# Kernel tuning notes

Hardware: AMD Instinct MI355X
Metric: run time of the kernel (lower is better)

## Reference

```python
import jax, jax.numpy as jnp
import numpy as np

N = 50000
NEG_SLOPE = 0.2  # PyG GATConv default negative_slope


def gat_conv(x, src, dst, W, a_src, a_dst, bias, concat):
    """One PyG-style GATConv (eval mode, self-loops already in src/dst).
    x: [N, F_in], W: [F_in, H*C], a_src/a_dst: [H, C], bias: [H*C] or [C].
    """
    H, C = a_src.shape
    xl = (x @ W).reshape(N, H, C)                      # [N, H, C]
    alpha_src = jnp.sum(xl * a_src, axis=-1)           # [N, H]
    alpha_dst = jnp.sum(xl * a_dst, axis=-1)           # [N, H]
    e = jax.nn.leaky_relu(alpha_src[src] + alpha_dst[dst], NEG_SLOPE)  # [E, H]
    # edge-softmax over incoming edges of each destination node
    m = jax.ops.segment_max(e, dst, num_segments=N)    # [N, H]
    e = jnp.exp(e - m[dst])
    s = jax.ops.segment_sum(e, dst, num_segments=N)    # [N, H]
    alpha = e / s[dst]                                 # [E, H]
    msg = xl[src] * alpha[:, :, None]                  # [E, H, C]
    out = jax.ops.segment_sum(msg, dst, num_segments=N)  # [N, H, C]
    out = out.reshape(N, H * C) if concat else out.mean(axis=1)
    return out + bias


def setup_inputs() -> dict:
    key = jax.random.key(0)
    ks = jax.random.split(key, 10)
    in_ch, hid, out_ch, heads = 128, 64, 64, 4
    E = 800000
    x = jax.random.normal(ks[0], (N, in_ch), dtype=jnp.float32)
    edge_index = jax.random.randint(ks[1], (2, E), 0, N, dtype=jnp.int64)
    s1 = 1.0 / np.sqrt(in_ch)
    s2 = 1.0 / np.sqrt(hid * heads)
    return {
        "x": x,
        "edge_index": edge_index,
        "W1": jax.random.normal(ks[2], (in_ch, heads * hid), jnp.float32) * s1,
        "att_src1": jax.random.normal(ks[3], (heads, hid), jnp.float32) * s1,
        "att_dst1": jax.random.normal(ks[4], (heads, hid), jnp.float32) * s1,
        "b1": jnp.zeros((heads * hid,), jnp.float32),
        "W2": jax.random.normal(ks[5], (heads * hid, out_ch), jnp.float32) * s2,
        "att_src2": jax.random.normal(ks[6], (1, out_ch), jnp.float32) * s2,
        "att_dst2": jax.random.normal(ks[7], (1, out_ch), jnp.float32) * s2,
        "b2": jnp.zeros((out_ch,), jnp.float32),
    }


def reference(x, edge_index, W1, att_src1, att_dst1, b1, W2, att_src2, att_dst2, b2):
    # PyG GATConv adds self-loops by default
    loops = jnp.arange(N, dtype=edge_index.dtype)
    src = jnp.concatenate([edge_index[0], loops])
    dst = jnp.concatenate([edge_index[1], loops])
    h = gat_conv(x, src, dst, W1, att_src1, att_dst1, b1, concat=True)
    h = jax.nn.elu(h)  # dropout is identity in eval mode
    out = gat_conv(h, src, dst, W2, att_src2, att_dst2, b2, concat=False)
    return out
```

## Files before the change

kernel.cpp:

```cpp
#include <hip/hip_runtime.h>
#include <math.h>


typedef unsigned short u16;
typedef short s8v __attribute__((ext_vector_type(8)));
typedef float f32x4 __attribute__((ext_vector_type(4)));

#define LOG2E 1.4426950408889634f

__device__ __forceinline__ float bflo(unsigned int u) {
  return __builtin_bit_cast(float, u << 16);
}
__device__ __forceinline__ float bfhi(unsigned int u) {
  return __builtin_bit_cast(float, u & 0xffff0000u);
}
__device__ __forceinline__ u16 f2bf(float f) {
  unsigned int u = __builtin_bit_cast(unsigned int, f);
  return (u16)((u + 0x7fff + ((u >> 16) & 1)) >> 16);
}


__global__ void prep_count_kernel(const int* __restrict__ ei, int E, int Nn,
                                  int* __restrict__ deg,
                                  const float* __restrict__ W1, u16* __restrict__ W1T,
                                  const float* __restrict__ W2, u16* __restrict__ W2T) {
  int i = blockIdx.x * blockDim.x + threadIdx.x;
  int Et = E + Nn;
  if (i < Et) {
    int dst = (i < E) ? ei[E + i] : (i - E);
    atomicAdd(&deg[dst], 1);
    return;
  }
  int e = i - Et;
  if (e < 128 * 256) {
    int k = e >> 8, n = e & 255;
    W1T[n * 128 + k] = f2bf(W1[e]);
    return;
  }
  e -= 128 * 256;
  if (e < 256 * 64) {
    int k = e >> 6, n = e & 63;
    W2T[n * 256 + k] = f2bf(W2[e]);
  }
}

__global__ void scan_partials_kernel(const int* __restrict__ deg,
                                     int* __restrict__ partials, int Ntot) {
  __shared__ int red[256];
  int t = threadIdx.x;
  int base = blockIdx.x * 1024 + t * 4;
  int s = 0;
  if (base + 3 < Ntot) {
    int4 v = *(const int4*)(deg + base);
    s = v.x + v.y + v.z + v.w;
  } else {
    for (int i = 0; i < 4; ++i)
      if (base + i < Ntot) s += deg[base + i];
  }
  red[t] = s;
  __syncthreads();
  for (int off = 128; off > 0; off >>= 1) {
    if (t < off) red[t] += red[t + off];
    __syncthreads();
  }
  if (t == 0) partials[blockIdx.x] = red[0];
}

__global__ void scan_final_kernel(const int* __restrict__ deg,
                                  const int* __restrict__ partials,
                                  int* __restrict__ rowptr,
                                  int* __restrict__ cursor, int Ntot, int NB) {
  __shared__ int sums[256];
  int t = threadIdx.x;
  int bid = blockIdx.x;
  int base = bid * 1024 + t * 4;
  int4 v = make_int4(0, 0, 0, 0);
  if (base + 3 < Ntot) {
    v = *(const int4*)(deg + base);
  } else {
    if (base + 0 < Ntot) v.x = deg[base + 0];
    if (base + 1 < Ntot) v.y = deg[base + 1];
    if (base + 2 < Ntot) v.z = deg[base + 2];
    if (base + 3 < Ntot) v.w = deg[base + 3];
  }
  sums[t] = v.x + v.y + v.z + v.w;
  __syncthreads();
  for (int off = 1; off < 256; off <<= 1) {
    int u = (t >= off) ? sums[t - off] : 0;
    __syncthreads();
    sums[t] += u;
    __syncthreads();
  }
  int boff = 0;
  for (int j = 0; j < bid; ++j) boff += partials[j];
  int excl = boff + ((t == 0) ? 0 : sums[t - 1]);
  int4 r;
  r.x = excl;
  r.y = r.x + v.x;
  r.z = r.y + v.y;
  r.w = r.z + v.z;
  if (base + 3 < Ntot) {
    *(int4*)(rowptr + base) = r;
    *(int4*)(cursor + base) = r;
  } else {
    if (base + 0 < Ntot) { rowptr[base + 0] = r.x; cursor[base + 0] = r.x; }
    if (base + 1 < Ntot) { rowptr[base + 1] = r.y; cursor[base + 1] = r.y; }
    if (base + 2 < Ntot) { rowptr[base + 2] = r.z; cursor[base + 2] = r.z; }
    if (base + 3 < Ntot) { rowptr[base + 3] = r.w; cursor[base + 3] = r.w; }
  }
}

__global__ void scatter_edges_kernel(const int* __restrict__ ei, int E, int Nn,
                                     int* __restrict__ cursor, int* __restrict__ col) {
  int e = blockIdx.x * blockDim.x + threadIdx.x;
  if (e >= E + Nn) return;
  int src, dst;
  if (e < E) { src = ei[e]; dst = ei[E + e]; }
  else       { src = dst = e - E; }
  int pos = atomicAdd(&cursor[dst], 1);
  col[pos] = src;
}


__global__ __launch_bounds__(256) void gemm1_fused_kernel(
    const float* __restrict__ x,
    const u16* __restrict__ w1t,
    const float* __restrict__ a_src,
    const float* __restrict__ a_dst,
    u16* __restrict__ C,
    float* __restrict__ asrc, float* __restrict__ adst,
    int M) {
  constexpr int BM = 128, BN = 128, BK = 32, PK = 40;
  __shared__ short As[BM][PK];
  __shared__ short Bs[BN][PK];
  int tid = threadIdx.x;
  int lane = tid & 63, w = tid >> 6;
  int q = lane >> 4, fr = lane & 15;
  int wm = (w >> 1) * 64, wn = (w & 1) * 64;
  int bm0 = blockIdx.x * BM, bn0 = blockIdx.y * BN;
  int fk = q * 8;

  f32x4 acc[4][4] = {};

  for (int k0 = 0; k0 < 128; k0 += BK) {
#pragma unroll
    for (int p = 0; p < 4; ++p) {
      int idx = p * 1024 + tid * 4;
      int r = idx >> 5, c = idx & 31;
      float4 v = make_float4(0.f, 0.f, 0.f, 0.f);
      if (bm0 + r < M) v = *(const float4*)(x + (size_t)(bm0 + r) * 128 + k0 + c);
      *(ushort4*)&As[r][c] = make_ushort4(f2bf(v.x), f2bf(v.y), f2bf(v.z), f2bf(v.w));
    }
#pragma unroll
    for (int p = 0; p < 2; ++p) {
      int idx = p * 2048 + tid * 8;
      int r = idx >> 5, c = idx & 31;
      *(s8v*)&Bs[r][c] = *(const s8v*)(w1t + (size_t)(bn0 + r) * 128 + k0 + c);
    }
    __syncthreads();

    s8v af[4], bf[4];
#pragma unroll
    for (int i = 0; i < 4; ++i)
      af[i] = *(const s8v*)&As[wm + i * 16 + fr][fk];
#pragma unroll
    for (int j = 0; j < 4; ++j)
      bf[j] = *(const s8v*)&Bs[wn + j * 16 + fr][fk];
#pragma unroll
    for (int i = 0; i < 4; ++i)
#pragma unroll
      for (int j = 0; j < 4; ++j)
        acc[i][j] = __builtin_amdgcn_mfma_f32_16x16x32_bf16(af[i], bf[j], acc[i][j], 0, 0, 0);
    __syncthreads();
  }

  int h = blockIdx.y * 2 + (wn >> 6);
  float asv[4], adv[4];
#pragma unroll
  for (int j = 0; j < 4; ++j) {
    asv[j] = a_src[h * 64 + j * 16 + fr];
    adv[j] = a_dst[h * 64 + j * 16 + fr];
  }
#pragma unroll
  for (int i = 0; i < 4; ++i) {
#pragma unroll
    for (int r = 0; r < 4; ++r) {
      int row = bm0 + wm + i * 16 + q * 4 + r;
      float ps = 0.f, pd = 0.f;
#pragma unroll
      for (int j = 0; j < 4; ++j) {
        ps = fmaf(acc[i][j][r], asv[j], ps);
        pd = fmaf(acc[i][j][r], adv[j], pd);
      }
#pragma unroll
      for (int mmask = 1; mmask < 16; mmask <<= 1) {
        ps += __shfl_xor(ps, mmask, 64);
        pd += __shfl_xor(pd, mmask, 64);
      }
      if (fr == 0 && row < M) {
        asrc[row * 4 + h] = ps * LOG2E;
        adst[row * 4 + h] = pd * LOG2E;
      }
    }
  }
#pragma unroll
  for (int i = 0; i < 4; ++i)
#pragma unroll
    for (int j = 0; j < 4; ++j)
#pragma unroll
      for (int r = 0; r < 4; ++r) {
        int row = bm0 + wm + i * 16 + q * 4 + r;
        if (row < M)
          C[(size_t)row * 256 + bn0 + wn + j * 16 + fr] = f2bf(acc[i][j][r]);
      }
}


__global__ __launch_bounds__(256) void gemm2_fused_kernel(
    const u16* __restrict__ A,
    const u16* __restrict__ Bt,
    const float* __restrict__ a_src,
    const float* __restrict__ a_dst,
    u16* __restrict__ C,
    float* __restrict__ asrc, float* __restrict__ adst,
    int M) {
  constexpr int BM = 128, BN = 64, BK = 32, PK = 40;
  __shared__ short As[BM][PK];
  __shared__ short Bs[BN][PK];
  __shared__ float alds[BM][4];
  int tid = threadIdx.x;
  int lane = tid & 63, w = tid >> 6;
  int q = lane >> 4, fr = lane & 15;
  int wm = (w >> 1) * 64, wn = (w & 1) * 32;
  int bm0 = blockIdx.x * BM;
  int fk = q * 8;

  f32x4 acc[4][2] = {};

  for (int k0 = 0; k0 < 256; k0 += BK) {
#pragma unroll
    for (int p = 0; p < 2; ++p) {
      int idx = p * 2048 + tid * 8;
      int r = idx / BK, c = idx % BK;
      *(s8v*)&As[r][c] = *(const s8v*)(A + (size_t)(bm0 + r) * 256 + k0 + c);
    }
    {
      int idx = tid * 8;
      int r = idx / BK, c = idx % BK;
      if (r < BN)
        *(s8v*)&Bs[r][c] = *(const s8v*)(Bt + (size_t)r * 256 + k0 + c);
    }
    __syncthreads();

    s8v af[4], bf[2];
#pragma unroll
    for (int i = 0; i < 4; ++i)
      af[i] = *(const s8v*)&As[wm + i * 16 + fr][fk];
#pragma unroll
    for (int j = 0; j < 2; ++j)
      bf[j] = *(const s8v*)&Bs[wn + j * 16 + fr][fk];
#pragma unroll
    for (int i = 0; i < 4; ++i)
#pragma unroll
      for (int j = 0; j < 2; ++j)
        acc[i][j] = __builtin_amdgcn_mfma_f32_16x16x32_bf16(af[i], bf[j], acc[i][j], 0, 0, 0);
    __syncthreads();
  }

  float asv[2], adv[2];
#pragma unroll
  for (int j = 0; j < 2; ++j) {
    asv[j] = a_src[wn + j * 16 + fr];
    adv[j] = a_dst[wn + j * 16 + fr];
  }
#pragma unroll
  for (int i = 0; i < 4; ++i) {
#pragma unroll
    for (int r = 0; r < 4; ++r) {
      int lr = wm + i * 16 + q * 4 + r;
      float ps = 0.f, pd = 0.f;
#pragma unroll
      for (int j = 0; j < 2; ++j) {
        ps = fmaf(acc[i][j][r], asv[j], ps);
        pd = fmaf(acc[i][j][r], adv[j], pd);
      }
#pragma unroll
      for (int mmask = 1; mmask < 16; mmask <<= 1) {
        ps += __shfl_xor(ps, mmask, 64);
        pd += __shfl_xor(pd, mmask, 64);
      }
      if (fr == 0) {
        alds[lr][(w & 1) * 2 + 0] = ps;
        alds[lr][(w & 1) * 2 + 1] = pd;
      }
    }
  }
#pragma unroll
  for (int i = 0; i < 4; ++i)
#pragma unroll
    for (int j = 0; j < 2; ++j)
#pragma unroll
      for (int r = 0; r < 4; ++r) {
        int row = bm0 + wm + i * 16 + q * 4 + r;
        if (row < M)
          C[(size_t)row * 64 + wn + j * 16 + fr] = f2bf(acc[i][j][r]);
      }
  __syncthreads();
  if (tid < BM) {
    int row = bm0 + tid;
    if (row < M) {
      asrc[row] = (alds[tid][0] + alds[tid][2]) * LOG2E;
      adst[row] = (alds[tid][1] + alds[tid][3]) * LOG2E;
    }
  }
}


__global__ void agg_multi_kernel(const u16* __restrict__ xlb,
                                 const float* __restrict__ asrc,
                                 const float* __restrict__ adst,
                                 const int* __restrict__ rowptr,
                                 const int* __restrict__ col,
                                 const float* __restrict__ bias,
                                 u16* __restrict__ hb, int Nn) {
  int n = blockIdx.x * 8 + (threadIdx.x >> 5);
  if (n >= Nn) return;
  int lane = threadIdx.x & 31;
  int h = lane >> 3;
  float adn = adst[n * 4 + h];
  int beg = rowptr[n], end = rowptr[n + 1];

  float s = 0.f;
  float acc[8] = {};

  float as0 = 0.f, as1 = 0.f, as2 = 0.f, as3 = 0.f;
  uint4 v0 = {}, v1 = {}, v2 = {}, v3 = {};
  {
    int sc = col[beg];
    as0 = asrc[sc * 4 + h];
    v0 = *(const uint4*)(xlb + (size_t)sc * 256 + lane * 8);
    if (beg + 1 < end) {
      int c1 = col[beg + 1];
      as1 = asrc[c1 * 4 + h];
      v1 = *(const uint4*)(xlb + (size_t)c1 * 256 + lane * 8);
    }
    if (beg + 2 < end) {
      int c2 = col[beg + 2];
      as2 = asrc[c2 * 4 + h];
      v2 = *(const uint4*)(xlb + (size_t)c2 * 256 + lane * 8);
    }
    if (beg + 3 < end) {
      int c3 = col[beg + 3];
      as3 = asrc[c3 * 4 + h];
      v3 = *(const uint4*)(xlb + (size_t)c3 * 256 + lane * 8);
    }
  }

  for (int i = beg; i < end; ++i) {
    float e = as0 + adn;
    e = fmaxf(e, 0.2f * e);
    uint4 vc = v0;
    as0 = as1; v0 = v1;
    as1 = as2; v1 = v2;
    as2 = as3; v2 = v3;
    if (i + 4 < end) {
      int sc = col[i + 4];
      as3 = asrc[sc * 4 + h];
      v3 = *(const uint4*)(xlb + (size_t)sc * 256 + lane * 8);
    }
    float w = __builtin_amdgcn_exp2f(e);
    s += w;
    acc[0] = fmaf(w, bflo(vc.x), acc[0]);
    acc[1] = fmaf(w, bfhi(vc.x), acc[1]);
    acc[2] = fmaf(w, bflo(vc.y), acc[2]);
    acc[3] = fmaf(w, bfhi(vc.y), acc[3]);
    acc[4] = fmaf(w, bflo(vc.z), acc[4]);
    acc[5] = fmaf(w, bfhi(vc.z), acc[5]);
    acc[6] = fmaf(w, bflo(vc.w), acc[6]);
    acc[7] = fmaf(w, bfhi(vc.w), acc[7]);
  }
  float inv_s = 1.f / s;

  float4 b0 = *(const float4*)(bias + lane * 8);
  float4 b1f = *(const float4*)(bias + lane * 8 + 4);
  float bb[8] = {b0.x, b0.y, b0.z, b0.w, b1f.x, b1f.y, b1f.z, b1f.w};
  u16 ov[8];
#pragma unroll
  for (int j = 0; j < 8; ++j) {
    float o = fmaf(acc[j], inv_s, bb[j]);
    o = (o > 0.f) ? o : __expf(o) - 1.f;
    ov[j] = f2bf(o);
  }
  *(uint4*)(hb + (size_t)n * 256 + lane * 8) = *(uint4*)ov;
}


__global__ void agg_single_kernel(const u16* __restrict__ xlb,
                                  const float* __restrict__ asrc,
                                  const float* __restrict__ adst,
                                  const int* __restrict__ rowptr,
                                  const int* __restrict__ col,
                                  const float* __restrict__ bias,
                                  float* __restrict__ out, int Nn) {
  int n = blockIdx.x * 32 + (threadIdx.x >> 3);
  if (n >= Nn) return;
  int lane = threadIdx.x & 7;
  float adn = adst[n];
  int beg = rowptr[n], end = rowptr[n + 1];

  float s = 0.f;
  float acc[8] = {};

  float as0 = 0.f, as1 = 0.f, as2 = 0.f;
  uint4 v0 = {}, v1 = {}, v2 = {};
  {
    int sc = col[beg];
    as0 = asrc[sc];
    v0 = *(const uint4*)(xlb + (size_t)sc * 64 + lane * 8);
    if (beg + 1 < end) {
      int c1 = col[beg + 1];
      as1 = asrc[c1];
      v1 = *(const uint4*)(xlb + (size_t)c1 * 64 + lane * 8);
    }
    if (beg + 2 < end) {
      int c2 = col[beg + 2];
      as2 = asrc[c2];
      v2 = *(const uint4*)(xlb + (size_t)c2 * 64 + lane * 8);
    }
  }

  for (int i = beg; i < end; ++i) {
    float e = as0 + adn;
    e = fmaxf(e, 0.2f * e);
    uint4 vc = v0;
    as0 = as1; v0 = v1;
    as1 = as2; v1 = v2;
    if (i + 3 < end) {
      int sc = col[i + 3];
      as2 = asrc[sc];
      v2 = *(const uint4*)(xlb + (size_t)sc * 64 + lane * 8);
    }
    float w = __builtin_amdgcn_exp2f(e);
    s += w;
    acc[0] = fmaf(w, bflo(vc.x), acc[0]);
    acc[1] = fmaf(w, bfhi(vc.x), acc[1]);
    acc[2] = fmaf(w, bflo(vc.y), acc[2]);
    acc[3] = fmaf(w, bfhi(vc.y), acc[3]);
    acc[4] = fmaf(w, bflo(vc.z), acc[4]);
    acc[5] = fmaf(w, bfhi(vc.z), acc[5]);
    acc[6] = fmaf(w, bflo(vc.w), acc[6]);
    acc[7] = fmaf(w, bfhi(vc.w), acc[7]);
  }
  float inv_s = 1.f / s;

  const float* bp = bias + lane * 8;
  float4 o0, o1;
  o0.x = fmaf(acc[0], inv_s, bp[0]);
  o0.y = fmaf(acc[1], inv_s, bp[1]);
  o0.z = fmaf(acc[2], inv_s, bp[2]);
  o0.w = fmaf(acc[3], inv_s, bp[3]);
  o1.x = fmaf(acc[4], inv_s, bp[4]);
  o1.y = fmaf(acc[5], inv_s, bp[5]);
  o1.z = fmaf(acc[6], inv_s, bp[6]);
  o1.w = fmaf(acc[7], inv_s, bp[7]);
  *(float4*)(out + (size_t)n * 64 + lane * 8) = o0;
  *(float4*)(out + (size_t)n * 64 + lane * 8 + 4) = o1;
}


extern "C" void kernel_launch(void* const* d_in, const int* in_sizes, int n_in,
                              void* d_out, int out_size, void* d_ws, size_t ws_size,
                              hipStream_t stream) {
  const float* x   = (const float*)d_in[0];
  const int*   ei  = (const int*)d_in[1];
  const float* W1  = (const float*)d_in[2];
  const float* as1 = (const float*)d_in[3];
  const float* ad1 = (const float*)d_in[4];
  const float* b1  = (const float*)d_in[5];
  const float* W2  = (const float*)d_in[6];
  const float* as2 = (const float*)d_in[7];
  const float* ad2 = (const float*)d_in[8];
  const float* b2  = (const float*)d_in[9];
  float* out = (float*)d_out;

  const int Nn = in_sizes[0] / 128;
  const int E  = in_sizes[1] / 2;
  const int Et = E + Nn;
  const int Ntot = Nn + 1;
  const int NB = (Ntot + 1023) / 1024;
  const int MB = (Nn + 127) / 128;
  const int Mpad = MB * 128;

  char* base = (char*)d_ws;
  size_t off = 0;
  auto alloc = [&](size_t bytes) -> void* {
    void* p = base + off;
    off = (off + bytes + 255) & ~(size_t)255;
    return p;
  };
  u16*   w1t      = (u16*)alloc((size_t)256 * 128 * 2);
  u16*   w2t      = (u16*)alloc((size_t)64 * 256 * 2);
  u16*   xlb1     = (u16*)alloc((size_t)Mpad * 256 * 2);
  u16*   hb       = (u16*)alloc((size_t)Mpad * 256 * 2);
  float* asrc1    = (float*)alloc((size_t)Nn * 4 * 4);
  float* adst1    = (float*)alloc((size_t)Nn * 4 * 4);
  float* asrc2    = (float*)alloc((size_t)Nn * 4);
  float* adst2    = (float*)alloc((size_t)Nn * 4);
  int*   deg      = (int*)alloc((size_t)(Ntot + 8) * 4);
  int*   rowptr   = (int*)alloc((size_t)(Ntot + 8) * 4);
  int*   cursor   = (int*)alloc((size_t)(Ntot + 8) * 4);
  int*   partials = (int*)alloc(256 * 4);
  int*   col      = (int*)alloc((size_t)Et * 4);
  u16*   xlb2     = xlb1;

  hipMemsetAsync(deg, 0, (size_t)Ntot * 4, stream);
  {
    int tot = Et + 128 * 256 + 256 * 64;
    prep_count_kernel<<<(tot + 255) / 256, 256, 0, stream>>>(
        ei, E, Nn, deg, W1, w1t, W2, w2t);
  }
  scan_partials_kernel<<<NB, 256, 0, stream>>>(deg, partials, Ntot);
  scan_final_kernel<<<NB, 256, 0, stream>>>(deg, partials, rowptr, cursor, Ntot, NB);
  scatter_edges_kernel<<<(Et + 255) / 256, 256, 0, stream>>>(ei, E, Nn, cursor, col);

  {
    dim3 grid(MB, 2);
    gemm1_fused_kernel<<<grid, 256, 0, stream>>>(x, w1t, as1, ad1, xlb1, asrc1, adst1, Nn);
  }
  agg_multi_kernel<<<(Nn + 7) / 8, 256, 0, stream>>>(xlb1, asrc1, adst1, rowptr, col, b1, hb, Nn);

  gemm2_fused_kernel<<<MB, 256, 0, stream>>>(hb, w2t, as2, ad2, xlb2, asrc2, adst2, Nn);
  agg_single_kernel<<<(Nn + 31) / 32, 256, 0, stream>>>(xlb2, asrc2, adst2, rowptr, col, b2, out, Nn);
}
```

Measured before the change: 245.5 us.

## Widen GEMM1 to full 256 columns, double GEMM2 K-tile, deepen agg prefetch

```diff
diff --git a/kernel.cpp b/kernel.cpp
--- a/kernel.cpp
+++ b/kernel.cpp
@@ -130,17 +130,17 @@
     u16* __restrict__ C,
     float* __restrict__ asrc, float* __restrict__ adst,
     int M) {
-  constexpr int BM = 128, BN = 128, BK = 32, PK = 40;
+  constexpr int BM = 128, BK = 32, PK = 40;
   __shared__ short As[BM][PK];
-  __shared__ short Bs[BN][PK];
+  __shared__ short Bs[256][PK];
   int tid = threadIdx.x;
   int lane = tid & 63, w = tid >> 6;
   int q = lane >> 4, fr = lane & 15;
-  int wm = (w >> 1) * 64, wn = (w & 1) * 64;
-  int bm0 = blockIdx.x * BM, bn0 = blockIdx.y * BN;
+  int wm = (w >> 1) * 64, wn = (w & 1) * 128;
+  int bm0 = blockIdx.x * BM;
   int fk = q * 8;
 
-  f32x4 acc[4][4] = {};
+  f32x4 acc[4][8] = {};
 
   for (int k0 = 0; k0 < 128; k0 += BK) {
 #pragma unroll
@@ -152,66 +152,72 @@
       *(ushort4*)&As[r][c] = make_ushort4(f2bf(v.x), f2bf(v.y), f2bf(v.z), f2bf(v.w));
     }
 #pragma unroll
-    for (int p = 0; p < 2; ++p) {
+    for (int p = 0; p < 4; ++p) {
       int idx = p * 2048 + tid * 8;
       int r = idx >> 5, c = idx & 31;
-      *(s8v*)&Bs[r][c] = *(const s8v*)(w1t + (size_t)(bn0 + r) * 128 + k0 + c);
-    }
-    __syncthreads();
-
-    s8v af[4], bf[4];
+      *(s8v*)&Bs[r][c] = *(const s8v*)(w1t + (size_t)r * 128 + k0 + c);
+    }
+    __syncthreads();
+
+    s8v af[4], bf[8];
 #pragma unroll
     for (int i = 0; i < 4; ++i)
       af[i] = *(const s8v*)&As[wm + i * 16 + fr][fk];
 #pragma unroll
-    for (int j = 0; j < 4; ++j)
+    for (int j = 0; j < 8; ++j)
       bf[j] = *(const s8v*)&Bs[wn + j * 16 + fr][fk];
 #pragma unroll
     for (int i = 0; i < 4; ++i)
 #pragma unroll
-      for (int j = 0; j < 4; ++j)
+      for (int j = 0; j < 8; ++j)
         acc[i][j] = __builtin_amdgcn_mfma_f32_16x16x32_bf16(af[i], bf[j], acc[i][j], 0, 0, 0);
     __syncthreads();
   }
 
-  int h = blockIdx.y * 2 + (wn >> 6);
-  float asv[4], adv[4];
-#pragma unroll
-  for (int j = 0; j < 4; ++j) {
-    asv[j] = a_src[h * 64 + j * 16 + fr];
-    adv[j] = a_dst[h * 64 + j * 16 + fr];
+  int h0 = wn >> 6;
+  float asv[8], adv[8];
+#pragma unroll
+  for (int j = 0; j < 8; ++j) {
+    asv[j] = a_src[wn + j * 16 + fr];
+    adv[j] = a_dst[wn + j * 16 + fr];
   }
 #pragma unroll
   for (int i = 0; i < 4; ++i) {
 #pragma unroll
     for (int r = 0; r < 4; ++r) {
       int row = bm0 + wm + i * 16 + q * 4 + r;
-      float ps = 0.f, pd = 0.f;
+      float ps0 = 0.f, pd0 = 0.f, ps1 = 0.f, pd1 = 0.f;
 #pragma unroll
       for (int j = 0; j < 4; ++j) {
-        ps = fmaf(acc[i][j][r], asv[j], ps);
-        pd = fmaf(acc[i][j][r], adv[j], pd);
+        ps0 = fmaf(acc[i][j][r], asv[j], ps0);
+        pd0 = fmaf(acc[i][j][r], adv[j], pd0);
+        ps1 = fmaf(acc[i][j + 4][r], asv[j + 4], ps1);
+        pd1 = fmaf(acc[i][j + 4][r], adv[j + 4], pd1);
       }
 #pragma unroll
       for (int mmask = 1; mmask < 16; mmask <<= 1) {
-        ps += __shfl_xor(ps, mmask, 64);
-        pd += __shfl_xor(pd, mmask, 64);
+        ps0 += __shfl_xor(ps0, mmask, 64);
+        pd0 += __shfl_xor(pd0, mmask, 64);
+        ps1 += __shfl_xor(ps1, mmask, 64);
+        pd1 += __shfl_xor(pd1, mmask, 64);
       }
       if (fr == 0 && row < M) {
-        asrc[row * 4 + h] = ps * LOG2E;
-        adst[row * 4 + h] = pd * LOG2E;
+        asrc[row * 4 + h0] = ps0 * LOG2E;
+        adst[row * 4 + h0] = pd0 * LOG2E;
+        asrc[row * 4 + h0 + 1] = ps1 * LOG2E;
+        adst[row * 4 + h0 + 1] = pd1 * LOG2E;
       }
     }
   }
 #pragma unroll
   for (int i = 0; i < 4; ++i)
 #pragma unroll
-    for (int j = 0; j < 4; ++j)
+    for (int j = 0; j < 8; ++j)
 #pragma unroll
       for (int r = 0; r < 4; ++r) {
         int row = bm0 + wm + i * 16 + q * 4 + r;
         if (row < M)
-          C[(size_t)row * 256 + bn0 + wn + j * 16 + fr] = f2bf(acc[i][j][r]);
+          C[(size_t)row * 256 + wn + j * 16 + fr] = f2bf(acc[i][j][r]);
       }
 }
 
@@ -224,7 +230,7 @@
     u16* __restrict__ C,
     float* __restrict__ asrc, float* __restrict__ adst,
     int M) {
-  constexpr int BM = 128, BN = 64, BK = 32, PK = 40;
+  constexpr int BM = 128, BN = 64, BK = 64, PK = 72;
   __shared__ short As[BM][PK];
   __shared__ short Bs[BN][PK];
   __shared__ float alds[BM][4];
@@ -239,31 +245,34 @@
 
   for (int k0 = 0; k0 < 256; k0 += BK) {
 #pragma unroll
+    for (int p = 0; p < 4; ++p) {
+      int idx = p * 2048 + tid * 8;
+      int r = idx / BK, c = idx % BK;
+      *(s8v*)&As[r][c] = *(const s8v*)(A + (size_t)(bm0 + r) * 256 + k0 + c);
+    }
+#pragma unroll
     for (int p = 0; p < 2; ++p) {
       int idx = p * 2048 + tid * 8;
       int r = idx / BK, c = idx % BK;
-      *(s8v*)&As[r][c] = *(const s8v*)(A + (size_t)(bm0 + r) * 256 + k0 + c);
-    }
-    {
-      int idx = tid * 8;
-      int r = idx / BK, c = idx % BK;
-      if (r < BN)
-        *(s8v*)&Bs[r][c] = *(const s8v*)(Bt + (size_t)r * 256 + k0 + c);
-    }
-    __syncthreads();
-
-    s8v af[4], bf[2];
-#pragma unroll
-    for (int i = 0; i < 4; ++i)
-      af[i] = *(const s8v*)&As[wm + i * 16 + fr][fk];
-#pragma unroll
-    for (int j = 0; j < 2; ++j)
-      bf[j] = *(const s8v*)&Bs[wn + j * 16 + fr][fk];
-#pragma unroll
-    for (int i = 0; i < 4; ++i)
+      *(s8v*)&Bs[r][c] = *(const s8v*)(Bt + (size_t)r * 256 + k0 + c);
+    }
+    __syncthreads();
+
+#pragma unroll
+    for (int ks = 0; ks < 2; ++ks) {
+      s8v af[4], bf[2];
+#pragma unroll
+      for (int i = 0; i < 4; ++i)
+        af[i] = *(const s8v*)&As[wm + i * 16 + fr][ks * 32 + fk];
 #pragma unroll
       for (int j = 0; j < 2; ++j)
-        acc[i][j] = __builtin_amdgcn_mfma_f32_16x16x32_bf16(af[i], bf[j], acc[i][j], 0, 0, 0);
+        bf[j] = *(const s8v*)&Bs[wn + j * 16 + fr][ks * 32 + fk];
+#pragma unroll
+      for (int i = 0; i < 4; ++i)
+#pragma unroll
+        for (int j = 0; j < 2; ++j)
+          acc[i][j] = __builtin_amdgcn_mfma_f32_16x16x32_bf16(af[i], bf[j], acc[i][j], 0, 0, 0);
+    }
     __syncthreads();
   }
 
@@ -411,8 +420,8 @@
   float s = 0.f;
   float acc[8] = {};
 
-  float as0 = 0.f, as1 = 0.f, as2 = 0.f;
-  uint4 v0 = {}, v1 = {}, v2 = {};
+  float as0 = 0.f, as1 = 0.f, as2 = 0.f, as3 = 0.f;
+  uint4 v0 = {}, v1 = {}, v2 = {}, v3 = {};
   {
     int sc = col[beg];
     as0 = asrc[sc];
@@ -427,6 +436,11 @@
       as2 = asrc[c2];
       v2 = *(const uint4*)(xlb + (size_t)c2 * 64 + lane * 8);
     }
+    if (beg + 3 < end) {
+      int c3 = col[beg + 3];
+      as3 = asrc[c3];
+      v3 = *(const uint4*)(xlb + (size_t)c3 * 64 + lane * 8);
+    }
   }
 
   for (int i = beg; i < end; ++i) {
@@ -435,10 +449,11 @@
     uint4 vc = v0;
     as0 = as1; v0 = v1;
     as1 = as2; v1 = v2;
-    if (i + 3 < end) {
-      int sc = col[i + 3];
-      as2 = asrc[sc];
-      v2 = *(const uint4*)(xlb + (size_t)sc * 64 + lane * 8);
+    as2 = as3; v2 = v3;
+    if (i + 4 < end) {
+      int sc = col[i + 4];
+      as3 = asrc[sc];
+      v3 = *(const uint4*)(xlb + (size_t)sc * 64 + lane * 8);
     }
     float w = __builtin_amdgcn_exp2f(e);
     s += w;
@@ -523,10 +538,7 @@
   scan_final_kernel<<<NB, 256, 0, stream>>>(deg, partials, rowptr, cursor, Ntot, NB);
   scatter_edges_kernel<<<(Et + 255) / 256, 256, 0, stream>>>(ei, E, Nn, cursor, col);
 
-  {
-    dim3 grid(MB, 2);
-    gemm1_fused_kernel<<<grid, 256, 0, stream>>>(x, w1t, as1, ad1, xlb1, asrc1, adst1, Nn);
-  }
+  gemm1_fused_kernel<<<MB, 256, 0, stream>>>(x, w1t, as1, ad1, xlb1, asrc1, adst1, Nn);
   agg_multi_kernel<<<(Nn + 7) / 8, 256, 0, stream>>>(xlb1, asrc1, adst1, rowptr, col, b1, hb, Nn);
 
   gemm2_fused_kernel<<<MB, 256, 0, stream>>>(hb, w2t, as2, ad2, xlb2, asrc2, adst2, Nn);
```

After: 255.5 us. 4.1% more time.
